# Performance work log

Hardware: AMD Instinct MI355X
Metric: run time of the kernel (lower is better)

The kernel has to match this reference:

```python
import jax, jax.numpy as jnp
import numpy as np

RQ_LEVELS = 4  # init_kwargs: rq_levels


def setup_inputs() -> dict:
    key = jax.random.key(0)
    kz, kc = jax.random.split(key)
    z = jax.random.normal(kz, (32768, 512), dtype=jnp.float32)
    cb = jax.random.normal(kc, (1024, 512), dtype=jnp.float32)
    cb = cb / jnp.linalg.norm(cb, axis=1, keepdims=True)  # F.normalize at init
    return {"z": z, "codebook": cb}


def reference(z, codebook):
    # z: [N, D]; codebook: [K, D]
    K = codebook.shape[0]
    cb_sq = jnp.sum(codebook ** 2, axis=1)  # [K]

    def step(carry, _):
        residual, qsum, closs, usage = carry
        # squared L2 distances: ||r||^2 - 2 r.c + ||c||^2  -> [N, K]
        d = jnp.sum(residual ** 2, axis=1, keepdims=True) - 2.0 * (residual @ codebook.T) + cb_sq[None, :]
        idx = jnp.argmin(d, axis=1)            # [N]
        q = codebook[idx]                      # embedding gather [N, D]
        closs = closs + jnp.mean((residual - jax.lax.stop_gradient(q)) ** 2)
        qsum = qsum + q
        residual = residual - q
        usage = usage + jnp.zeros((K,), jnp.float32).at[idx].add(1.0)  # bincount
        return (residual, qsum, closs, usage), idx

    init = (z, jnp.zeros_like(z), jnp.zeros((), z.dtype), jnp.zeros((K,), jnp.float32))
    (_, qsum, closs, usage), idxs = jax.lax.scan(step, init, None, length=RQ_LEVELS)
    discrete_codes = idxs.T                    # [N, rq_levels]
    z_quantized = z + jax.lax.stop_gradient(qsum - z)  # straight-through
    return z_quantized, closs, discrete_codes, usage
```

## Files before the change

### kernel.cpp

```cpp
#include <hip/hip_runtime.h>

#define NROWS  32768
#define KCODES 1024
#define DDIM   512
#define LEVELS 4

#define CLOSS_OFF (NROWS * DDIM)
#define CODES_OFF (CLOSS_OFF + 1)
#define USAGE_OFF (CODES_OFF + NROWS * LEVELS)

typedef __attribute__((ext_vector_type(8))) short bf16x8;
typedef __attribute__((ext_vector_type(4))) float f32x4;
typedef __attribute__((ext_vector_type(8))) unsigned short u16x8;

__device__ __forceinline__ unsigned short bf16_rn(float f) {
  unsigned int u = __float_as_uint(f);
  return (unsigned short)((u + 0x7FFFu + ((u >> 16) & 1u)) >> 16);
}
__device__ __forceinline__ float bf16_f(unsigned short h) {
  return __uint_as_float(((unsigned int)h) << 16);
}
__device__ __forceinline__ void gload16(const void* g, void* l) {
  __builtin_amdgcn_global_load_lds(
      (const __attribute__((address_space(1))) unsigned int*)g,
      (__attribute__((address_space(3))) unsigned int*)l, 16, 0, 0);
}

__global__ __launch_bounds__(256) void prep_kernel(const float* __restrict__ in,
                                                   float* __restrict__ Rout,
                                                   unsigned short* __restrict__ hi,
                                                   unsigned short* __restrict__ lo,
                                                   int nrows) {
  __shared__ float buf[4][DDIM];
  const int wid  = threadIdx.x >> 6;
  const int lane = threadIdx.x & 63;
  const int row  = blockIdx.x * 4 + wid;
  if (row >= nrows) return;
  const float4* src = reinterpret_cast<const float4*>(in + (size_t)row * DDIM);
  float vals[8];
#pragma unroll
  for (int t = 0; t < 2; ++t) {
    const float4 v = src[lane * 2 + t];
    *reinterpret_cast<float4*>(&buf[wid][lane * 8 + t * 4]) = v;
    vals[t * 4 + 0] = v.x; vals[t * 4 + 1] = v.y;
    vals[t * 4 + 2] = v.z; vals[t * 4 + 3] = v.w;
  }
  u16x8 hh, ll;
#pragma unroll
  for (int e = 0; e < 8; ++e) {
    const unsigned short h = bf16_rn(vals[e]);
    hh[e] = h;
    ll[e] = bf16_rn(__fsub_rn(vals[e], bf16_f(h)));
  }
  const int pos = (lane & 56) | ((lane & 7) ^ (row & 7));
  *reinterpret_cast<u16x8*>(&hi[(size_t)row * DDIM + pos * 8]) = hh;
  *reinterpret_cast<u16x8*>(&lo[(size_t)row * DDIM + pos * 8]) = ll;
  float chain = 0.0f;
  if (lane < 32) {
    const int base = (lane >> 3) * 128 + (lane & 7);
    float a = buf[wid][base];
    chain = __fmul_rn(a, a);
#pragma unroll
    for (int t = 1; t < 16; ++t) {
      a = buf[wid][base + 8 * t];
      chain = __fadd_rn(chain, __fmul_rn(a, a));
    }
  }
  chain = __fadd_rn(chain, __shfl_xor(chain, 1));
  chain = __fadd_rn(chain, __shfl_xor(chain, 2));
  chain = __fadd_rn(chain, __shfl_xor(chain, 4));
  chain = __fadd_rn(chain, __shfl_xor(chain, 8));
  chain = __fadd_rn(chain, __shfl_xor(chain, 16));
  if (lane == 0) Rout[row] = chain;
}

__global__ __launch_bounds__(512) void gemm_topk_kernel(
    const unsigned short* __restrict__ Ahi, const unsigned short* __restrict__ Alo,
    const unsigned short* __restrict__ Bhi, const unsigned short* __restrict__ Blo,
    const float* __restrict__ Rrow, const float* __restrict__ cbsq,
    unsigned int* __restrict__ keys) {
  __shared__ short ring[3][24576];
  __shared__ unsigned int trip[8][64][3];
  const int tid  = threadIdx.x;
  const int lane = tid & 63;
  const int wid  = tid >> 6;
  const int wm = wid >> 1, wn = wid & 1;
  const int c = lane & 15, q = lane >> 4;
  const int p = blockIdx.x;
  const int rg  = (p >> 6) * 8 + (p & 7);
  const int cbk = (p >> 3) & 7;
  const int rowBase = rg * 256;
  const int colBase = cbk * 128;

  float4 R4[4];
  float cq[4];
#pragma unroll
  for (int rf = 0; rf < 4; ++rf)
    R4[rf] = *reinterpret_cast<const float4*>(&Rrow[rowBase + wm * 64 + rf * 16 + q * 4]);
#pragma unroll
  for (int cf = 0; cf < 4; ++cf)
    cq[cf] = cbsq[colBase + wn * 64 + cf * 16 + c];

  f32x4 acc[4][4];
#pragma unroll
  for (int rf = 0; rf < 4; ++rf)
#pragma unroll
    for (int cf = 0; cf < 4; ++cf) acc[rf][cf] = (f32x4)0.0f;

  const char* const Asrc[3] = {(const char*)Ahi, (const char*)Ahi, (const char*)Alo};
  const char* const Bsrc[3] = {(const char*)Bhi, (const char*)Blo, (const char*)Bhi};
  const int laneOff = (lane >> 3) * 1024 + (lane & 7) * 16;

  auto STAGE_A = [&](int t, int l) {
    const int g = wid + 8 * l;
    const char* src = Asrc[t >> 3] + (size_t)(rowBase + g * 8) * 1024 + (t & 7) * 128 + laneOff;
    gload16(src, &ring[t % 3][g * 512]);
  };
  auto STAGE_B = [&](int t, int l) {
    const int g = wid + 8 * l;
    const char* src = Bsrc[t >> 3] + (size_t)(colBase + g * 8) * 1024 + (t & 7) * 128 + laneOff;
    gload16(src, &ring[t % 3][16384 + g * 512]);
  };

#pragma unroll
  for (int l = 0; l < 4; ++l) STAGE_A(0, l);
#pragma unroll
  for (int l = 0; l < 2; ++l) STAGE_B(0, l);
#pragma unroll
  for (int l = 0; l < 4; ++l) STAGE_A(1, l);
#pragma unroll
  for (int l = 0; l < 2; ++l) STAGE_B(1, l);
  asm volatile("s_waitcnt vmcnt(6)" ::: "memory");
  __builtin_amdgcn_s_barrier();
  __builtin_amdgcn_sched_barrier(0);

  for (int t = 0; t < 24; ++t) {
    const short* As = &ring[t % 3][0];
    const short* Bs = &ring[t % 3][16384];
#pragma unroll
    for (int kh = 0; kh < 2; ++kh) {
      const int ch = ((kh * 4 + q) ^ (c & 7)) * 8;
      bf16x8 ar[4], br[4];
#pragma unroll
      for (int rf = 0; rf < 4; ++rf)
        ar[rf] = *reinterpret_cast<const bf16x8*>(&As[(wm * 64 + rf * 16 + c) * 64 + ch]);
#pragma unroll
      for (int cf = 0; cf < 4; ++cf)
        br[cf] = *reinterpret_cast<const bf16x8*>(&Bs[(wn * 64 + cf * 16 + c) * 64 + ch]);
      if (t + 2 < 24) {
        if (kh == 0) { STAGE_A(t + 2, 0); STAGE_A(t + 2, 1); STAGE_B(t + 2, 0); }
        else         { STAGE_A(t + 2, 2); STAGE_A(t + 2, 3); STAGE_B(t + 2, 1); }
      }
      __builtin_amdgcn_s_barrier();
      __builtin_amdgcn_sched_barrier(0);
      __builtin_amdgcn_s_setprio(1);
#pragma unroll
      for (int rf = 0; rf < 4; ++rf)
#pragma unroll
        for (int cf = 0; cf < 4; ++cf)
          acc[rf][cf] = __builtin_amdgcn_mfma_f32_16x16x32_bf16(ar[rf], br[cf], acc[rf][cf], 0, 0, 0);
      __builtin_amdgcn_s_setprio(0);
      if (kh == 1) {
        if (t == 22)      asm volatile("s_waitcnt vmcnt(0)" ::: "memory");
        else if (t < 22)  asm volatile("s_waitcnt vmcnt(6)" ::: "memory");
      }
      __builtin_amdgcn_s_barrier();
      __builtin_amdgcn_sched_barrier(0);
    }
  }

#pragma unroll
  for (int rf = 0; rf < 4; ++rf) {
#pragma unroll
    for (int jj = 0; jj < 4; ++jj) {
      const float Rv = (jj == 0) ? R4[rf].x : (jj == 1) ? R4[rf].y : (jj == 2) ? R4[rf].z : R4[rf].w;
      unsigned int v[4];
#pragma unroll
      for (int cf = 0; cf < 4; ++cf) {
        float d = __fadd_rn(__fsub_rn(Rv, __fmul_rn(2.0f, acc[rf][cf][jj])), cq[cf]);
        d = fmaxf(d, 0.0f);
        v[cf] = (__float_as_uint(d) & 0xFFFFFF80u) | (unsigned int)(wn * 64 + cf * 16 + c);
      }
      const unsigned int m01 = min(v[0], v[1]), M01 = max(v[0], v[1]);
      const unsigned int m23 = min(v[2], v[3]), M23 = max(v[2], v[3]);
      unsigned int s0 = min(m01, m23);
      const unsigned int x = max(m01, m23), mM = min(M01, M23);
      unsigned int s1 = min(x, mM);
      unsigned int s2 = min(max(x, mM), max(M01, M23));
#pragma unroll
      for (int m = 1; m < 16; m <<= 1) {
        const unsigned int t0 = (unsigned int)__shfl_xor((int)s0, m);
        const unsigned int t1 = (unsigned int)__shfl_xor((int)s1, m);
        const unsigned int t2 = (unsigned int)__shfl_xor((int)s2, m);
        const unsigned int bb = max(s0, t0), aa = min(s1, t1);
        const unsigned int r0 = min(s0, t0);
        const unsigned int r1 = min(bb, aa);
        const unsigned int r2 = min(max(bb, aa), min(s2, t2));
        s0 = r0; s1 = r1; s2 = r2;
      }
      if (c == 0) {
        const int lrow = rf * 16 + q * 4 + jj;
        trip[wid][lrow][0] = s0;
        trip[wid][lrow][1] = s1;
        trip[wid][lrow][2] = s2;
      }
    }
  }
  __syncthreads();
  if ((wid & 1) == 0) {
    const unsigned int a0 = trip[wid][lane][0], a1 = trip[wid][lane][1], a2 = trip[wid][lane][2];
    const unsigned int b0 = trip[wid + 1][lane][0], b1 = trip[wid + 1][lane][1], b2 = trip[wid + 1][lane][2];
    const unsigned int bb = max(a0, b0), aa = min(a1, b1);
    const unsigned int s0 = min(a0, b0);
    const unsigned int s1 = min(bb, aa);
    const unsigned int s2 = min(max(bb, aa), min(a2, b2));
    const int row = rowBase + wm * 64 + lane;
    unsigned int* kp = keys + (size_t)row * 24 + cbk * 3;
    kp[0] = s0; kp[1] = s1; kp[2] = s2;
  }
}

__global__ __launch_bounds__(256) void level_finish_kernel(
    const unsigned int* __restrict__ keys, const float* rin, float* rout,
    const float* __restrict__ cb, const float* __restrict__ cbsq,
    float* __restrict__ Rrow, float* __restrict__ usage,
    float* __restrict__ codes, unsigned short* __restrict__ Ahi,
    unsigned short* __restrict__ Alo, int level, int do_split) {
  __shared__ float buf[4][DDIM];
  const int wid  = threadIdx.x >> 6;
  const int lane = threadIdx.x & 63;
  const int row  = blockIdx.x * 4 + wid;

  const unsigned int k = (lane < 24) ? keys[(size_t)row * 24 + lane] : 0xFFFFFFFFu;
  const int mycode = (lane < 24) ? ((lane / 3) * 128 + (int)(k & 127u)) : 0x7FFFFFFF;
  const float Rv_old = Rrow[row];
  unsigned int g = k;
#pragma unroll
  for (int m = 1; m < 64; m <<= 1) g = min(g, (unsigned int)__shfl_xor((int)g, m));
  const float dmin = __uint_as_float(g & 0xFFFFFF80u);
  const float W = 0.010f + 5.0e-4f * sqrtf(Rv_old);
  const bool cand = (lane < 24) && (__uint_as_float(k & 0xFFFFFF80u) <= dmin + W);
  const unsigned long long mask = __ballot(cand);
  int winner;
  if (__popcll(mask) == 1) {
    int w = cand ? mycode : 0x7FFFFFFF;
#pragma unroll
    for (int m = 1; m < 64; m <<= 1) w = min(w, __shfl_xor(w, m));
    winner = w;
  } else {
    float db = __builtin_inff();
    int   ib = 0x7FFFFFFF;
    if (cand) {
      const float4* rr = reinterpret_cast<const float4*>(rin + (size_t)row * DDIM);
      const float4* cc = reinterpret_cast<const float4*>(cb + (size_t)mycode * DDIM);
      float pp = 0.0f;
      for (int t = 0; t < DDIM / 4; ++t) {
        const float4 a = rr[t], b = cc[t];
        pp = fmaf(a.x, b.x, pp); pp = fmaf(a.y, b.y, pp);
        pp = fmaf(a.z, b.z, pp); pp = fmaf(a.w, b.w, pp);
      }
      db = __fadd_rn(__fsub_rn(Rv_old, __fmul_rn(2.0f, pp)), cbsq[mycode]);
      ib = mycode;
    }
#pragma unroll
    for (int m = 1; m < 64; m <<= 1) {
      const float od = __shfl_xor(db, m);
      const int   oi = __shfl_xor(ib, m);
      if (od < db || (od == db && oi < ib)) { db = od; ib = oi; }
    }
    winner = ib;
  }

  const float4* r4 = reinterpret_cast<const float4*>(rin + (size_t)row * DDIM) + lane * 2;
  const float4* q4 = reinterpret_cast<const float4*>(cb + (size_t)winner * DDIM) + lane * 2;
  float4* o4 = reinterpret_cast<float4*>(rout + (size_t)row * DDIM) + lane * 2;
  float vals[8];
#pragma unroll
  for (int t = 0; t < 2; ++t) {
    float4 r = r4[t], qv = q4[t], o;
    o.x = __fsub_rn(r.x, qv.x);
    o.y = __fsub_rn(r.y, qv.y);
    o.z = __fsub_rn(r.z, qv.z);
    o.w = __fsub_rn(r.w, qv.w);
    o4[t] = o;
    *reinterpret_cast<float4*>(&buf[wid][lane * 8 + t * 4]) = o;
    vals[t * 4 + 0] = o.x; vals[t * 4 + 1] = o.y;
    vals[t * 4 + 2] = o.z; vals[t * 4 + 3] = o.w;
  }
  if (do_split) {
    u16x8 hh, ll;
#pragma unroll
    for (int e = 0; e < 8; ++e) {
      const unsigned short h = bf16_rn(vals[e]);
      hh[e] = h;
      ll[e] = bf16_rn(__fsub_rn(vals[e], bf16_f(h)));
    }
    const int pos = (lane & 56) | ((lane & 7) ^ (row & 7));
    *reinterpret_cast<u16x8*>(&Ahi[(size_t)row * DDIM + pos * 8]) = hh;
    *reinterpret_cast<u16x8*>(&Alo[(size_t)row * DDIM + pos * 8]) = ll;
  }
  float chain = 0.0f;
  if (lane < 32) {
    const int base = (lane >> 3) * 128 + (lane & 7);
    float a = buf[wid][base];
    chain = __fmul_rn(a, a);
#pragma unroll
    for (int t = 1; t < 16; ++t) {
      a = buf[wid][base + 8 * t];
      chain = __fadd_rn(chain, __fmul_rn(a, a));
    }
  }
  chain = __fadd_rn(chain, __shfl_xor(chain, 1));
  chain = __fadd_rn(chain, __shfl_xor(chain, 2));
  chain = __fadd_rn(chain, __shfl_xor(chain, 4));
  chain = __fadd_rn(chain, __shfl_xor(chain, 8));
  chain = __fadd_rn(chain, __shfl_xor(chain, 16));
  if (lane == 0) {
    Rrow[row] = chain;
    atomicAdd(&usage[winner], 1.0f);
    codes[(size_t)row * LEVELS + level] = (float)winner;
  }
}

#define BM 64
#define BN 256
#define DT 32
#define LDP (DT + 4)

__global__ __launch_bounds__(256) void argmin_kernel(const float* __restrict__ res,
                                                     const float* __restrict__ cb,
                                                     const float* __restrict__ Rr_,
                                                     const float* __restrict__ cbsq,
                                                     float* __restrict__ codes,
                                                     int level) {
  __shared__ float As_[BM][LDP];
  __shared__ float Bs_[BN][LDP];
  const int tid = threadIdx.x;
  const int tx = tid & 15;
  const int ty = tid >> 4;
  const size_t brow = (size_t)blockIdx.x * BM;
  float minv[4]; int mini[4]; float Rv[4];
#pragma unroll
  for (int i = 0; i < 4; ++i) { minv[i] = __builtin_inff(); mini[i] = 0; Rv[i] = Rr_[brow + ty + 16 * i]; }
  for (int nc = 0; nc < KCODES; nc += BN) {
    float acc[4][16];
#pragma unroll
    for (int i = 0; i < 4; ++i)
#pragma unroll
      for (int j = 0; j < 16; ++j) acc[i][j] = 0.0f;
    for (int dt = 0; dt < DDIM; dt += DT) {
      __syncthreads();
#pragma unroll
      for (int qq = 0; qq < 2; ++qq) {
        const int ff = tid + qq * 256; const int r = ff >> 3; const int seg = (ff & 7) * 4;
        *reinterpret_cast<float4*>(&As_[r][seg]) =
            *reinterpret_cast<const float4*>(&res[(brow + r) * DDIM + dt + seg]);
      }
#pragma unroll
      for (int qq = 0; qq < 8; ++qq) {
        const int ff = tid + qq * 256; const int r = ff >> 3; const int seg = (ff & 7) * 4;
        *reinterpret_cast<float4*>(&Bs_[r][seg]) =
            *reinterpret_cast<const float4*>(&cb[(size_t)(nc + r) * DDIM + dt + seg]);
      }
      __syncthreads();
#pragma unroll
      for (int dd = 0; dd < DT; dd += 4) {
        float4 av[4];
#pragma unroll
        for (int i = 0; i < 4; ++i) av[i] = *reinterpret_cast<const float4*>(&As_[ty + 16 * i][dd]);
#pragma unroll
        for (int j = 0; j < 16; ++j) {
          const float4 bv = *reinterpret_cast<const float4*>(&Bs_[tx + 16 * j][dd]);
#pragma unroll
          for (int i = 0; i < 4; ++i) {
            acc[i][j] = fmaf(av[i].x, bv.x, acc[i][j]);
            acc[i][j] = fmaf(av[i].y, bv.y, acc[i][j]);
            acc[i][j] = fmaf(av[i].z, bv.z, acc[i][j]);
            acc[i][j] = fmaf(av[i].w, bv.w, acc[i][j]);
          }
        }
      }
    }
#pragma unroll
    for (int j = 0; j < 16; ++j) {
      const int code = nc + tx + 16 * j;
      const float cq = cbsq[code];
#pragma unroll
      for (int i = 0; i < 4; ++i) {
        const float dist = __fadd_rn(__fsub_rn(Rv[i], __fmul_rn(2.0f, acc[i][j])), cq);
        if (dist < minv[i]) { minv[i] = dist; mini[i] = code; }
      }
    }
  }
#pragma unroll
  for (int m = 1; m < 16; m <<= 1) {
#pragma unroll
    for (int i = 0; i < 4; ++i) {
      const float ov = __shfl_xor(minv[i], m);
      const int   oi = __shfl_xor(mini[i], m);
      if (ov < minv[i] || (ov == minv[i] && oi < mini[i])) { minv[i] = ov; mini[i] = oi; }
    }
  }
  if (tx == 0) {
#pragma unroll
    for (int i = 0; i < 4; ++i)
      codes[(brow + ty + 16 * i) * LEVELS + level] = (float)mini[i];
  }
}

__global__ __launch_bounds__(256) void sub_split_rowsq_kernel(
    const float* rin, float* rout, const float* __restrict__ cb,
    const float* __restrict__ codes, float* __restrict__ usage,
    float* __restrict__ Rout, int level) {
  __shared__ float buf[4][DDIM];
  const int wid  = threadIdx.x >> 6;
  const int lane = threadIdx.x & 63;
  const int row  = blockIdx.x * 4 + wid;
  const int idx = (int)codes[(size_t)row * LEVELS + level];
  const float4* r4 = reinterpret_cast<const float4*>(rin + (size_t)row * DDIM) + lane * 2;
  const float4* q4 = reinterpret_cast<const float4*>(cb + (size_t)idx * DDIM) + lane * 2;
  float4* o4 = reinterpret_cast<float4*>(rout + (size_t)row * DDIM) + lane * 2;
#pragma unroll
  for (int t = 0; t < 2; ++t) {
    float4 r = r4[t], q = q4[t], o;
    o.x = __fsub_rn(r.x, q.x);
    o.y = __fsub_rn(r.y, q.y);
    o.z = __fsub_rn(r.z, q.z);
    o.w = __fsub_rn(r.w, q.w);
    o4[t] = o;
    *reinterpret_cast<float4*>(&buf[wid][lane * 8 + t * 4]) = o;
  }
  float chain = 0.0f;
  if (lane < 32) {
    const int base = (lane >> 3) * 128 + (lane & 7);
    float a = buf[wid][base];
    chain = __fmul_rn(a, a);
#pragma unroll
    for (int t = 1; t < 16; ++t) {
      a = buf[wid][base + 8 * t];
      chain = __fadd_rn(chain, __fmul_rn(a, a));
    }
  }
  chain = __fadd_rn(chain, __shfl_xor(chain, 1));
  chain = __fadd_rn(chain, __shfl_xor(chain, 2));
  chain = __fadd_rn(chain, __shfl_xor(chain, 4));
  chain = __fadd_rn(chain, __shfl_xor(chain, 8));
  chain = __fadd_rn(chain, __shfl_xor(chain, 16));
  if (lane == 0) {
    Rout[row] = chain;
    atomicAdd(&usage[idx], 1.0f);
  }
}

__global__ __launch_bounds__(256) void sumR_kernel(const float* __restrict__ R,
                                                   float* __restrict__ slot) {
  const int t = blockIdx.x * 256 + threadIdx.x;
  float s = 0.0f;
#pragma unroll
  for (int k = 0; k < 4; ++k) s += R[t + k * 8192];
#pragma unroll
  for (int m = 1; m < 64; m <<= 1) s += __shfl_xor(s, m);
  __shared__ float ws[4];
  if ((threadIdx.x & 63) == 0) ws[threadIdx.x >> 6] = s;
  __syncthreads();
  if (threadIdx.x == 0) atomicAdd(slot, ((ws[0] + ws[1]) + (ws[2] + ws[3])));
}

__global__ __launch_bounds__(256) void finalize_zq_kernel(const float* __restrict__ z,
                                                          const float* __restrict__ cb,
                                                          const float* __restrict__ codes,
                                                          float* __restrict__ zq) {
  const int row  = (int)((blockIdx.x * 256 + threadIdx.x) >> 6);
  const int lane = threadIdx.x & 63;
  int c[4];
#pragma unroll
  for (int l = 0; l < 4; ++l) c[l] = (int)codes[(size_t)row * LEVELS + l];
#pragma unroll
  for (int t = 0; t < 2; ++t) {
    const int o = lane * 8 + t * 4;
    float4 s = *reinterpret_cast<const float4*>(&cb[(size_t)c[0] * DDIM + o]);
#pragma unroll
    for (int l = 1; l < 4; ++l) {
      const float4 q = *reinterpret_cast<const float4*>(&cb[(size_t)c[l] * DDIM + o]);
      s.x = __fadd_rn(s.x, q.x);
      s.y = __fadd_rn(s.y, q.y);
      s.z = __fadd_rn(s.z, q.z);
      s.w = __fadd_rn(s.w, q.w);
    }
    const float4 zz = *reinterpret_cast<const float4*>(&z[(size_t)row * DDIM + o]);
    float4 r;
    r.x = __fadd_rn(zz.x, __fsub_rn(s.x, zz.x));
    r.y = __fadd_rn(zz.y, __fsub_rn(s.y, zz.y));
    r.z = __fadd_rn(zz.z, __fsub_rn(s.z, zz.z));
    r.w = __fadd_rn(zz.w, __fsub_rn(s.w, zz.w));
    *reinterpret_cast<float4*>(&zq[(size_t)row * DDIM + o]) = r;
  }
}

__global__ void closs_final_kernel(const float* __restrict__ acc, float* __restrict__ out) {
  if (threadIdx.x == 0 && blockIdx.x == 0) {
    float c = 0.0f;
#pragma unroll
    for (int l = 0; l < 4; ++l)
      c = __fadd_rn(c, __fmul_rn(acc[l], 0x1p-24f));
    out[0] = c;
  }
}

extern "C" void kernel_launch(void* const* d_in, const int* in_sizes, int n_in,
                              void* d_out, int out_size, void* d_ws, size_t ws_size,
                              hipStream_t stream) {
  const float* z  = (const float*)d_in[0];
  const float* cb = (const float*)d_in[1];
  float* out   = (float*)d_out;
  float* zq    = out;
  float* closs = out + CLOSS_OFF;
  float* codes = out + CODES_OFF;
  float* usage = out + USAGE_OFF;

  float* R    = (float*)d_ws;
  float* cbsq = R + NROWS;
  float* cacc = cbsq + KCODES;

  const size_t WS_NEED = (size_t)(NROWS + KCODES + 4) * 4
                       + (size_t)NROWS * 24 * 4
                       + 2ull * KCODES * DDIM * 2
                       + 2ull * NROWS * DDIM * 2;

  hipMemsetAsync(usage, 0, KCODES * sizeof(float), stream);
  hipMemsetAsync(cacc, 0, LEVELS * sizeof(float), stream);

  if (ws_size >= WS_NEED) {
    unsigned int*   keys = (unsigned int*)(cacc + 4);
    unsigned short* Bhi  = (unsigned short*)(keys + (size_t)NROWS * 24);
    unsigned short* Blo  = Bhi + (size_t)KCODES * DDIM;
    unsigned short* Ahi  = Blo + (size_t)KCODES * DDIM;
    unsigned short* Alo  = Ahi + (size_t)NROWS * DDIM;

    prep_kernel<<<NROWS / 4, 256, 0, stream>>>(z, R, Ahi, Alo, NROWS);
    prep_kernel<<<KCODES / 4, 256, 0, stream>>>(cb, cbsq, Bhi, Blo, KCODES);

    for (int l = 0; l < LEVELS; ++l) {
      const float* res = (l == 0) ? z : zq;
      gemm_topk_kernel<<<1024, 512, 0, stream>>>(Ahi, Alo, Bhi, Blo, R, cbsq, keys);
      level_finish_kernel<<<NROWS / 4, 256, 0, stream>>>(keys, res, zq, cb, cbsq, R,
                                                         usage, codes, Ahi, Alo, l,
                                                         (l < 3) ? 1 : 0);
      sumR_kernel<<<32, 256, 0, stream>>>(R, cacc + l);
    }
  } else {
    prep_kernel<<<NROWS / 4, 256, 0, stream>>>(z, R, (unsigned short*)(cacc + 4),
                                               (unsigned short*)(cacc + 4) + NROWS, NROWS);
    prep_kernel<<<KCODES / 4, 256, 0, stream>>>(cb, cbsq, (unsigned short*)(cacc + 4),
                                                (unsigned short*)(cacc + 4) + KCODES, KCODES);
    for (int l = 0; l < LEVELS; ++l) {
      const float* res = (l == 0) ? z : zq;
      argmin_kernel<<<NROWS / BM, 256, 0, stream>>>(res, cb, R, cbsq, codes, l);
      sub_split_rowsq_kernel<<<NROWS / 4, 256, 0, stream>>>(res, zq, cb, codes, usage, R, l);
      sumR_kernel<<<32, 256, 0, stream>>>(R, cacc + l);
    }
  }

  finalize_zq_kernel<<<NROWS / 4, 256, 0, stream>>>(z, cb, codes, zq);
  closs_final_kernel<<<1, 64, 0, stream>>>(cacc, closs);
}
```

Baseline: 819.5 us.

## Shrink GEMM tile to 128 rows with double buffering and two blocks per CU

The distance GEMM block changes from 512 threads on a 256x128 tile with a 3-stage LDS ring to 256 threads on a 128x128 tile with a 2-stage ring and two blocks per CU. Each stage now loads both K-halves into registers before issuing the next prefetch, then runs all MFMAs and waits, which drops the per-half barriers. The last level also skips writing the residual, which is never read afterwards. This trades per-block prefetch depth and the finer-grained barrier interleave for more resident blocks and less LDS per block, and the full vmcnt(0) wait each iteration may expose memory latency.

Measured after the change: 926.0 us. +13.0%, slower.

```diff
diff --git a/kernel.cpp b/kernel.cpp
--- a/kernel.cpp
+++ b/kernel.cpp
@@ -74,13 +74,13 @@
   if (lane == 0) Rout[row] = chain;
 }
 
-__global__ __launch_bounds__(512) void gemm_topk_kernel(
+__global__ __launch_bounds__(256, 2) void gemm_topk_kernel(
     const unsigned short* __restrict__ Ahi, const unsigned short* __restrict__ Alo,
     const unsigned short* __restrict__ Bhi, const unsigned short* __restrict__ Blo,
     const float* __restrict__ Rrow, const float* __restrict__ cbsq,
     unsigned int* __restrict__ keys) {
-  __shared__ short ring[3][24576];
-  __shared__ unsigned int trip[8][64][3];
+  __shared__ short ring[2][16384];
+  __shared__ unsigned int trip[4][64][3];
   const int tid  = threadIdx.x;
   const int lane = tid & 63;
   const int wid  = tid >> 6;
@@ -89,7 +89,7 @@
   const int p = blockIdx.x;
   const int rg  = (p >> 6) * 8 + (p & 7);
   const int cbk = (p >> 3) & 7;
-  const int rowBase = rg * 256;
+  const int rowBase = rg * 128;
   const int colBase = cbk * 128;
 
   float4 R4[4];
@@ -111,59 +111,50 @@
   const char* const Bsrc[3] = {(const char*)Bhi, (const char*)Blo, (const char*)Bhi};
   const int laneOff = (lane >> 3) * 1024 + (lane & 7) * 16;
 
-  auto STAGE_A = [&](int t, int l) {
-    const int g = wid + 8 * l;
-    const char* src = Asrc[t >> 3] + (size_t)(rowBase + g * 8) * 1024 + (t & 7) * 128 + laneOff;
-    gload16(src, &ring[t % 3][g * 512]);
+  auto STAGE = [&](int t) {
+    const char* Ab = Asrc[t >> 3];
+    const char* Bb = Bsrc[t >> 3];
+    const int seg = (t & 7) * 128;
+    short* dst = &ring[t & 1][0];
+#pragma unroll
+    for (int l = 0; l < 4; ++l) {
+      const int g = wid + 4 * l;
+      gload16(Ab + (size_t)(rowBase + g * 8) * 1024 + seg + laneOff, dst + g * 512);
+      gload16(Bb + (size_t)(colBase + g * 8) * 1024 + seg + laneOff, dst + 8192 + g * 512);
+    }
   };
-  auto STAGE_B = [&](int t, int l) {
-    const int g = wid + 8 * l;
-    const char* src = Bsrc[t >> 3] + (size_t)(colBase + g * 8) * 1024 + (t & 7) * 128 + laneOff;
-    gload16(src, &ring[t % 3][16384 + g * 512]);
-  };
-
-#pragma unroll
-  for (int l = 0; l < 4; ++l) STAGE_A(0, l);
-#pragma unroll
-  for (int l = 0; l < 2; ++l) STAGE_B(0, l);
-#pragma unroll
-  for (int l = 0; l < 4; ++l) STAGE_A(1, l);
-#pragma unroll
-  for (int l = 0; l < 2; ++l) STAGE_B(1, l);
-  asm volatile("s_waitcnt vmcnt(6)" ::: "memory");
+
+  STAGE(0);
+  asm volatile("s_waitcnt vmcnt(0)" ::: "memory");
   __builtin_amdgcn_s_barrier();
   __builtin_amdgcn_sched_barrier(0);
 
   for (int t = 0; t < 24; ++t) {
-    const short* As = &ring[t % 3][0];
-    const short* Bs = &ring[t % 3][16384];
+    const short* As = &ring[t & 1][0];
+    const short* Bs = &ring[t & 1][8192];
+    bf16x8 ar[2][4], br[2][4];
 #pragma unroll
     for (int kh = 0; kh < 2; ++kh) {
       const int ch = ((kh * 4 + q) ^ (c & 7)) * 8;
-      bf16x8 ar[4], br[4];
 #pragma unroll
       for (int rf = 0; rf < 4; ++rf)
-        ar[rf] = *reinterpret_cast<const bf16x8*>(&As[(wm * 64 + rf * 16 + c) * 64 + ch]);
+        ar[kh][rf] = *reinterpret_cast<const bf16x8*>(&As[(wm * 64 + rf * 16 + c) * 64 + ch]);
 #pragma unroll
       for (int cf = 0; cf < 4; ++cf)
-        br[cf] = *reinterpret_cast<const bf16x8*>(&Bs[(wn * 64 + cf * 16 + c) * 64 + ch]);
-      if (t + 2 < 24) {
-        if (kh == 0) { STAGE_A(t + 2, 0); STAGE_A(t + 2, 1); STAGE_B(t + 2, 0); }
-        else         { STAGE_A(t + 2, 2); STAGE_A(t + 2, 3); STAGE_B(t + 2, 1); }
-      }
-      __builtin_amdgcn_s_barrier();
-      __builtin_amdgcn_sched_barrier(0);
-      __builtin_amdgcn_s_setprio(1);
+        br[kh][cf] = *reinterpret_cast<const bf16x8*>(&Bs[(wn * 64 + cf * 16 + c) * 64 + ch]);
+    }
+    if (t + 1 < 24) STAGE(t + 1);
+    __builtin_amdgcn_s_setprio(1);
+#pragma unroll
+    for (int kh = 0; kh < 2; ++kh)
 #pragma unroll
       for (int rf = 0; rf < 4; ++rf)
 #pragma unroll
         for (int cf = 0; cf < 4; ++cf)
-          acc[rf][cf] = __builtin_amdgcn_mfma_f32_16x16x32_bf16(ar[rf], br[cf], acc[rf][cf], 0, 0, 0);
-      __builtin_amdgcn_s_setprio(0);
-      if (kh == 1) {
-        if (t == 22)      asm volatile("s_waitcnt vmcnt(0)" ::: "memory");
-        else if (t < 22)  asm volatile("s_waitcnt vmcnt(6)" ::: "memory");
-      }
+          acc[rf][cf] = __builtin_amdgcn_mfma_f32_16x16x32_bf16(ar[kh][rf], br[kh][cf], acc[rf][cf], 0, 0, 0);
+    __builtin_amdgcn_s_setprio(0);
+    if (t + 1 < 24) {
+      asm volatile("s_waitcnt vmcnt(0)" ::: "memory");
       __builtin_amdgcn_s_barrier();
       __builtin_amdgcn_sched_barrier(0);
     }
@@ -214,7 +205,7 @@
     const unsigned int s0 = min(a0, b0);
     const unsigned int s1 = min(bb, aa);
     const unsigned int s2 = min(max(bb, aa), min(a2, b2));
-    const int row = rowBase + wm * 64 + lane;
+    const int row = rowBase + (wid >> 1) * 64 + lane;
     unsigned int* kp = keys + (size_t)row * 24 + cbk * 3;
     kp[0] = s0; kp[1] = s1; kp[2] = s2;
   }
@@ -225,7 +216,7 @@
     const float* __restrict__ cb, const float* __restrict__ cbsq,
     float* __restrict__ Rrow, float* __restrict__ usage,
     float* __restrict__ codes, unsigned short* __restrict__ Ahi,
-    unsigned short* __restrict__ Alo, int level, int do_split) {
+    unsigned short* __restrict__ Alo, int level, int do_split, int do_write) {
   __shared__ float buf[4][DDIM];
   const int wid  = threadIdx.x >> 6;
   const int lane = threadIdx.x & 63;
@@ -282,7 +273,7 @@
     o.y = __fsub_rn(r.y, qv.y);
     o.z = __fsub_rn(r.z, qv.z);
     o.w = __fsub_rn(r.w, qv.w);
-    o4[t] = o;
+    if (do_write) o4[t] = o;
     *reinterpret_cast<float4*>(&buf[wid][lane * 8 + t * 4]) = o;
     vals[t * 4 + 0] = o.x; vals[t * 4 + 1] = o.y;
     vals[t * 4 + 2] = o.z; vals[t * 4 + 3] = o.w;
@@ -542,9 +533,10 @@
 
     for (int l = 0; l < LEVELS; ++l) {
       const float* res = (l == 0) ? z : zq;
-      gemm_topk_kernel<<<1024, 512, 0, stream>>>(Ahi, Alo, Bhi, Blo, R, cbsq, keys);
+      gemm_topk_kernel<<<2048, 256, 0, stream>>>(Ahi, Alo, Bhi, Blo, R, cbsq, keys);
       level_finish_kernel<<<NROWS / 4, 256, 0, stream>>>(keys, res, zq, cb, cbsq, R,
                                                          usage, codes, Ahi, Alo, l,
+                                                         (l < 3) ? 1 : 0,
                                                          (l < 3) ? 1 : 0);
       sumR_kernel<<<32, 256, 0, stream>>>(R, cacc + l);
     }
```
